# Performance work log

Hardware: AMD Instinct MI355X
Metric: run time of the kernel (lower is better)

## Reference

```python
import jax, jax.numpy as jnp
import numpy as np

N_NODES = 50000
N_EDGES = 1600000
SLOPE = 0.01  # LeakyReLU default negative slope


def _leaky(x):
    return jnp.where(x >= 0, x, SLOPE * x)


def _gcn(x, W, b, row, col, num_nodes):
    """PyG GCNConv: x' = D^{-1/2}(A+I)D^{-1/2} X W + b (self-loops already in row/col)."""
    x = x @ W  # [N, 64]
    deg = jax.ops.segment_sum(jnp.ones_like(row, dtype=x.dtype), col, num_segments=num_nodes)
    dinv = jnp.where(deg > 0, jax.lax.rsqrt(deg), 0.0)
    norm = dinv[row] * dinv[col]  # [E+N]
    msg = x[row] * norm[:, None]  # gather + scale, [E+N, 64]
    out = jax.ops.segment_sum(msg, col, num_segments=num_nodes)
    return out + b


def setup_inputs() -> dict:
    key = jax.random.key(0)
    ks = jax.random.split(key, 24)
    d = {}
    d["screen"] = jax.random.normal(ks[0], (N_NODES, 768), jnp.float32)
    d["des"] = jax.random.normal(ks[1], (N_NODES, 768), jnp.float32)
    d["tweet"] = jax.random.normal(ks[2], (N_NODES, 768), jnp.float32)
    d["profile"] = jax.random.normal(ks[3], (N_NODES, 5), jnp.float32)
    d["personal"] = jax.random.normal(ks[4], (N_NODES, 7), jnp.float32)
    d["edge"] = jax.random.randint(ks[5], (2, N_EDGES), 0, N_NODES, dtype=jnp.int32)

    def lin(k, fan_in, fan_out):
        s = 1.0 / np.sqrt(fan_in)
        k1, k2 = jax.random.split(k)
        W = jax.random.uniform(k1, (fan_in, fan_out), jnp.float32, -s, s)
        b = jax.random.uniform(k2, (fan_out,), jnp.float32, -s, s)
        return W, b

    d["W_screen"], d["b_screen"] = lin(ks[6], 768, 16)
    d["W_des"], d["b_des"] = lin(ks[7], 768, 16)
    d["W_tweet"], d["b_tweet"] = lin(ks[8], 768, 16)
    d["W_pro"], d["b_pro"] = lin(ks[9], 5, 8)
    d["W_per"], d["b_per"] = lin(ks[10], 7, 8)
    d["W_lin"], d["b_lin"] = lin(ks[11], 64, 64)
    d["W_g1"], d["b_g1"] = lin(ks[12], 64, 64)
    d["W_g2"], d["b_g2"] = lin(ks[13], 64, 64)
    d["W_g3"], d["b_g3"] = lin(ks[14], 64, 64)
    d["W_o1"], d["b_o1"] = lin(ks[15], 64, 64)
    d["W_o2"], d["b_o2"] = lin(ks[16], 64, 2)
    return d


def reference(screen, des, tweet, profile, personal, edge,
              W_screen, b_screen, W_des, b_des, W_tweet, b_tweet,
              W_pro, b_pro, W_per, b_per, W_lin, b_lin,
              W_g1, b_g1, W_g2, b_g2, W_g3, b_g3,
              W_o1, b_o1, W_o2, b_o2):
    n = screen.shape[0]
    # dropout layers act as identity in eval mode
    s = _leaky(screen @ W_screen + b_screen)
    de = _leaky(des @ W_des + b_des)
    t = _leaky(tweet @ W_tweet + b_tweet)
    p = _leaky(profile @ W_pro + b_pro)
    pe = _leaky(personal @ W_per + b_per)
    x1 = jnp.concatenate((s, de, t, p, pe), axis=1)  # [N, 64]
    x = _leaky(x1 @ W_lin + b_lin)
    # add self-loops once (shared by all three GCN layers)
    loops = jnp.arange(n, dtype=edge.dtype)
    row = jnp.concatenate([edge[0], loops])
    col = jnp.concatenate([edge[1], loops])
    x = _gcn(x, W_g1, b_g1, row, col, n) + x1
    x = _gcn(x, W_g2, b_g2, row, col, n) + x1
    x = _gcn(x, W_g3, b_g3, row, col, n) + x1
    x = _leaky(x @ W_o1 + b_o1)
    return jax.nn.sigmoid(x @ W_o2 + b_o2)
```

## Files before the change

### kernel.cpp

```cpp
#include <hip/hip_runtime.h>

__device__ __forceinline__ float leaky(float v) { return v >= 0.f ? v : 0.01f * v; }

__device__ __forceinline__ void fma4(float4& a, float s, const float4& w) {
    a.x = fmaf(s, w.x, a.x); a.y = fmaf(s, w.y, a.y);
    a.z = fmaf(s, w.z, a.z); a.w = fmaf(s, w.w, a.w);
}

__device__ __forceinline__ unsigned short f2bf(float x) {
    unsigned b = __float_as_uint(x);
    return (unsigned short)((b + 0x7FFFu + ((b >> 16) & 1u)) >> 16);
}
__device__ __forceinline__ float bf2f(unsigned short u) {
    return __uint_as_float(((unsigned)u) << 16);
}

typedef __attribute__((ext_vector_type(8))) short short8v;
typedef __attribute__((ext_vector_type(4))) float float4v;

__global__ void k_deg(const int* __restrict__ col, int E, int* __restrict__ deg) {
    int e = blockIdx.x * blockDim.x + threadIdx.x;
    if (e < E) atomicAdd(&deg[col[e]], 1);
}

__global__ __launch_bounds__(256) void k_scan_part(const int* __restrict__ deg,
                                                   int* __restrict__ part,
                                                   int* __restrict__ bsum, int N) {
    __shared__ int tmp[256];
    int tid = threadIdx.x;
    int i = blockIdx.x * 256 + tid;
    int v = (i < N) ? deg[i] : 0;
    tmp[tid] = v;
    __syncthreads();
    for (int ofs = 1; ofs < 256; ofs <<= 1) {
        int t = (tid >= ofs) ? tmp[tid - ofs] : 0;
        __syncthreads();
        tmp[tid] += t;
        __syncthreads();
    }
    int incl = tmp[tid];
    if (i < N) part[i] = incl - v;
    if (tid == 255) bsum[blockIdx.x] = incl;
}

__global__ __launch_bounds__(256) void k_scan_sums(const int* __restrict__ bsum,
                                                   int* __restrict__ boff, int NB,
                                                   int* __restrict__ offs_last) {
    __shared__ int tmp[256];
    int tid = threadIdx.x;
    int v = (tid < NB) ? bsum[tid] : 0;
    tmp[tid] = v;
    __syncthreads();
    for (int ofs = 1; ofs < 256; ofs <<= 1) {
        int t = (tid >= ofs) ? tmp[tid - ofs] : 0;
        __syncthreads();
        tmp[tid] += t;
        __syncthreads();
    }
    int incl = tmp[tid];
    if (tid < NB) boff[tid] = incl - v;
    if (tid == 255) offs_last[0] = incl;
}

__global__ __launch_bounds__(256) void k_scan_final(const int* __restrict__ part,
                                                    const int* __restrict__ boff,
                                                    const int* __restrict__ deg,
                                                    int* __restrict__ offs,
                                                    int* __restrict__ pos,
                                                    float* __restrict__ dinv, int N) {
    int i = blockIdx.x * 256 + threadIdx.x;
    if (i < N) {
        int o = part[i] + boff[blockIdx.x];
        offs[i] = o;
        pos[i] = o;
        dinv[i] = rsqrtf((float)(deg[i] + 1));
    }
}

__global__ void k_fill(const int* __restrict__ row, const int* __restrict__ col, int E,
                       int* __restrict__ pos, int* __restrict__ csr) {
    int e = blockIdx.x * blockDim.x + threadIdx.x;
    if (e < E) {
        int p = atomicAdd(&pos[col[e]], 1);
        csr[p] = row[e];
    }
}

__global__ __launch_bounds__(512) void k_featB(
    const float* __restrict__ s, const float* __restrict__ d, const float* __restrict__ t,
    const float* __restrict__ Ws, const float* __restrict__ bs2,
    const float* __restrict__ Wd, const float* __restrict__ bd2,
    const float* __restrict__ Wt, const float* __restrict__ bt2,
    const float* __restrict__ prof, const float* __restrict__ pers,
    const float* __restrict__ Wp, const float* __restrict__ bp,
    const float* __restrict__ Wpe, const float* __restrict__ bpe,
    float* __restrict__ x1g, int N, int NG) {
    __shared__ short8v wfv[3072];

    const int bid = blockIdx.x;
    const int tid = threadIdx.x;

    if (bid >= 3 * NG) {
        int n = (bid - 3 * NG) * 512 + tid;
        if (n >= N) return;
        float pv[5], pe[7];
#pragma unroll
        for (int i = 0; i < 5; ++i) pv[i] = prof[(size_t)n * 5 + i];
#pragma unroll
        for (int i = 0; i < 7; ++i) pe[i] = pers[(size_t)n * 7 + i];
        float o[16];
#pragma unroll
        for (int j = 0; j < 8; ++j) {
            float a = bp[j];
#pragma unroll
            for (int i = 0; i < 5; ++i) a = fmaf(pv[i], Wp[i * 8 + j], a);
            o[j] = leaky(a);
            float a2 = bpe[j];
#pragma unroll
            for (int i = 0; i < 7; ++i) a2 = fmaf(pe[i], Wpe[i * 8 + j], a2);
            o[8 + j] = leaky(a2);
        }
#pragma unroll
        for (int v = 0; v < 4; ++v)
            *reinterpret_cast<float4*>(x1g + (size_t)n * 64 + 48 + v * 4) =
                make_float4(o[v * 4], o[v * 4 + 1], o[v * 4 + 2], o[v * 4 + 3]);
        return;
    }

    const int f = bid / NG;
    const int grp = bid - f * NG;
    const float* __restrict__ X = (f == 0) ? s : ((f == 1) ? d : t);
    const float* __restrict__ W = (f == 0) ? Ws : ((f == 1) ? Wd : Wt);
    const float* __restrict__ B = (f == 0) ? bs2 : ((f == 1) ? bd2 : bt2);
    const int n0 = grp * 128;
    const int lane = tid & 63;
    const int wid = tid >> 6;

    short* wfs = (short*)wfv;
#pragma unroll
    for (int v = 0; v < 6; ++v) {
        int idx4 = tid + v * 512;
        float4 w4 = *reinterpret_cast<const float4*>(W + (size_t)idx4 * 4);
        int k = idx4 >> 2;
        int j0 = (idx4 & 3) * 4;
        int c = k >> 5, g = (k >> 3) & 3, i = k & 7;
        float wq[4] = {w4.x, w4.y, w4.z, w4.w};
#pragma unroll
        for (int q = 0; q < 4; ++q) {
            int sl = (c * 64 + g * 16 + j0 + q) * 8 + i;
            unsigned short h = f2bf(wq[q]);
            wfs[sl] = (short)h;
            wfs[12288 + sl] = (short)f2bf(wq[q] - bf2f(h));
        }
    }
    __syncthreads();

    const int nb = n0 + wid * 16;
    int mrow = nb + (lane & 15); if (mrow >= N) mrow = N - 1;
    const float* base = X + (size_t)mrow * 768 + ((lane >> 4) << 3);

    float4 pa[4], pb[4];
#pragma unroll
    for (int u = 0; u < 4; ++u) {
        pa[u] = *reinterpret_cast<const float4*>(base + u * 32);
        pb[u] = *reinterpret_cast<const float4*>(base + u * 32 + 4);
    }
    float4v acc = {0.f, 0.f, 0.f, 0.f};

#pragma unroll
    for (int c = 0; c < 24; ++c) {
        const int u = c & 3;
        float xs[8] = {pa[u].x, pa[u].y, pa[u].z, pa[u].w,
                       pb[u].x, pb[u].y, pb[u].z, pb[u].w};
        if (c + 4 < 24) {
            pa[u] = *reinterpret_cast<const float4*>(base + (c + 4) * 32);
            pb[u] = *reinterpret_cast<const float4*>(base + (c + 4) * 32 + 4);
        }
        short8v xh, xl;
#pragma unroll
        for (int i = 0; i < 8; ++i) {
            unsigned short h = f2bf(xs[i]);
            xh[i] = (short)h;
            xl[i] = (short)f2bf(xs[i] - bf2f(h));
        }
        short8v wh = wfv[c * 64 + lane];
        short8v wl = wfv[1536 + c * 64 + lane];
        acc = __builtin_amdgcn_mfma_f32_16x16x32_bf16(xh, wh, acc, 0, 0, 0);
        acc = __builtin_amdgcn_mfma_f32_16x16x32_bf16(xl, wh, acc, 0, 0, 0);
        acc = __builtin_amdgcn_mfma_f32_16x16x32_bf16(xh, wl, acc, 0, 0, 0);
    }

    int j = lane & 15;
    float bb = B[j];
#pragma unroll
    for (int r = 0; r < 4; ++r) {
        int n = nb + ((lane >> 4) << 2) + r;
        if (n < N) x1g[(size_t)n * 64 + f * 16 + j] = leaky(acc[r] + bb);
    }
}

__global__ __launch_bounds__(256, 4) void k_mm64(const float* __restrict__ xin,
                                                 const float* __restrict__ W,
                                                 const float* __restrict__ bias,
                                                 const float* __restrict__ dinvv,
                                                 int act, int tobf16,
                                                 void* __restrict__ outp, int N) {
    __shared__ float4 xt4[1024];
    __shared__ float4 wt4[1024];
    const int tid = threadIdx.x;
    const int n0 = blockIdx.x * 64;
#pragma unroll
    for (int v = 0; v < 4; ++v) {
        int L = v * 256 + tid;
        int n = L >> 4, c4 = L & 15;
        int nn = n0 + n; if (nn >= N) nn = N - 1;
        xt4[n * 16 + (c4 ^ (n & 15))] = *reinterpret_cast<const float4*>(xin + (size_t)nn * 64 + c4 * 4);
        wt4[L] = *reinterpret_cast<const float4*>(W + (size_t)L * 4);
    }
    __syncthreads();
    const int nq = tid & 15;
    const int jq = tid >> 4;
    float4 acc[4];
#pragma unroll
    for (int g = 0; g < 4; ++g) acc[g] = make_float4(0.f, 0.f, 0.f, 0.f);
    for (int k = 0; k < 64; k += 4) {
        float4 w0 = wt4[(k + 0) * 16 + jq];
        float4 w1 = wt4[(k + 1) * 16 + jq];
        float4 w2 = wt4[(k + 2) * 16 + jq];
        float4 w3 = wt4[(k + 3) * 16 + jq];
        int k4 = k >> 2;
#pragma unroll
        for (int g = 0; g < 4; ++g) {
            int n = nq + (g << 4);
            float4 xv = xt4[n * 16 + (k4 ^ (n & 15))];
            fma4(acc[g], xv.x, w0);
            fma4(acc[g], xv.y, w1);
            fma4(acc[g], xv.z, w2);
            fma4(acc[g], xv.w, w3);
        }
    }
    float4 bb = make_float4(0.f, 0.f, 0.f, 0.f);
    if (bias) bb = *reinterpret_cast<const float4*>(bias + jq * 4);
#pragma unroll
    for (int g = 0; g < 4; ++g) {
        int n = nq + (g << 4);
        if (n0 + n >= N) continue;
        float4 r = acc[g];
        r.x += bb.x; r.y += bb.y; r.z += bb.z; r.w += bb.w;
        if (act) { r.x = leaky(r.x); r.y = leaky(r.y); r.z = leaky(r.z); r.w = leaky(r.w); }
        if (dinvv) {
            float dv = dinvv[n0 + n];
            r.x *= dv; r.y *= dv; r.z *= dv; r.w *= dv;
        }
        if (tobf16) {
            ushort4 o;
            o.x = f2bf(r.x); o.y = f2bf(r.y); o.z = f2bf(r.z); o.w = f2bf(r.w);
            *reinterpret_cast<ushort4*>((unsigned short*)outp + (size_t)(n0 + n) * 64 + jq * 4) = o;
        } else {
            *reinterpret_cast<float4*>((float*)outp + (size_t)(n0 + n) * 64 + jq * 4) = r;
        }
    }
}

__global__ __launch_bounds__(256) void k_agg(const unsigned short* __restrict__ z,
                                             const int* __restrict__ offs,
                                             const int* __restrict__ csr,
                                             const float* __restrict__ dinv,
                                             const float* __restrict__ bias,
                                             const float* __restrict__ x1,
                                             float* __restrict__ xout, int N) {
    int lane = threadIdx.x & 63;
    int c = blockIdx.x * 4 + (threadIdx.x >> 6);
    if (c >= N) return;
    int s = __builtin_amdgcn_readfirstlane(offs[c]);
    int e = __builtin_amdgcn_readfirstlane(offs[c + 1]);
    const unsigned short* zl = z + lane;
    float acc = bf2f(zl[(size_t)c * 64]);
    float a0 = 0.f, a1 = 0.f, a2 = 0.f, a3 = 0.f;
    float a4 = 0.f, a5 = 0.f, a6 = 0.f, a7 = 0.f;
    int j = s;
    for (; j + 8 <= e; j += 8) {
        int r0 = csr[j + 0], r1 = csr[j + 1], r2 = csr[j + 2], r3 = csr[j + 3];
        int r4 = csr[j + 4], r5 = csr[j + 5], r6 = csr[j + 6], r7 = csr[j + 7];
        a0 += bf2f(zl[(size_t)r0 * 64]);
        a1 += bf2f(zl[(size_t)r1 * 64]);
        a2 += bf2f(zl[(size_t)r2 * 64]);
        a3 += bf2f(zl[(size_t)r3 * 64]);
        a4 += bf2f(zl[(size_t)r4 * 64]);
        a5 += bf2f(zl[(size_t)r5 * 64]);
        a6 += bf2f(zl[(size_t)r6 * 64]);
        a7 += bf2f(zl[(size_t)r7 * 64]);
    }
    for (; j < e; ++j) acc += bf2f(zl[(size_t)csr[j] * 64]);
    acc += ((a0 + a1) + (a2 + a3)) + ((a4 + a5) + (a6 + a7));
    xout[(size_t)c * 64 + lane] = dinv[c] * acc + bias[lane] + x1[(size_t)c * 64 + lane];
}

__global__ __launch_bounds__(256) void k_head(const float* __restrict__ xin,
                                              const float* __restrict__ Wo1,
                                              const float* __restrict__ bo1,
                                              const float* __restrict__ Wo2,
                                              const float* __restrict__ bo2,
                                              float* __restrict__ out, int N) {
    __shared__ float xsg[64][65];
    __shared__ float wg[64][65];
    __shared__ float hs[64][65];
    __shared__ float wo2[128];
    const int tid = threadIdx.x;
    const int n0 = blockIdx.x * 64;
#pragma unroll
    for (int v = 0; v < 4; ++v) {
        int idx = tid + v * 256;
        int n = idx >> 4;
        int jj = (idx & 15) << 2;
        float4 xv = make_float4(0.f, 0.f, 0.f, 0.f);
        if (n0 + n < N) xv = *reinterpret_cast<const float4*>(xin + (size_t)(n0 + n) * 64 + jj);
        xsg[n][jj] = xv.x; xsg[n][jj + 1] = xv.y; xsg[n][jj + 2] = xv.z; xsg[n][jj + 3] = xv.w;
        float4 w = *reinterpret_cast<const float4*>(Wo1 + (size_t)n * 64 + jj);
        wg[n][jj] = w.x; wg[n][jj + 1] = w.y; wg[n][jj + 2] = w.z; wg[n][jj + 3] = w.w;
    }
    if (tid < 128) wo2[tid] = Wo2[tid];
    __syncthreads();
    int j = tid & 63;
    int g = tid >> 6;
    float bj = bo1[j];
    for (int i = 0; i < 16; ++i) {
        int n = g * 16 + i;
        float a = bj;
#pragma unroll
        for (int k = 0; k < 64; ++k) a += xsg[n][k] * wg[k][j];
        hs[n][j] = leaky(a);
    }
    __syncthreads();
    if (tid < 128) {
        int n = tid >> 1;
        int j2 = tid & 1;
        float a = bo2[j2];
#pragma unroll
        for (int k = 0; k < 64; ++k) a += hs[n][k] * wo2[k * 2 + j2];
        if (n0 + n < N) out[(size_t)(n0 + n) * 2 + j2] = 1.f / (1.f + expf(-a));
    }
}

extern "C" void kernel_launch(void* const* d_in, const int* in_sizes, int n_in,
                              void* d_out, int out_size, void* d_ws, size_t ws_size,
                              hipStream_t stream) {
    const float* screen   = (const float*)d_in[0];
    const float* des      = (const float*)d_in[1];
    const float* tweet    = (const float*)d_in[2];
    const float* profile  = (const float*)d_in[3];
    const float* personal = (const float*)d_in[4];
    const int*   edge     = (const int*)d_in[5];
    const float* Ws  = (const float*)d_in[6],  *bs  = (const float*)d_in[7];
    const float* Wd  = (const float*)d_in[8],  *bd  = (const float*)d_in[9];
    const float* Wt  = (const float*)d_in[10], *bt  = (const float*)d_in[11];
    const float* Wp  = (const float*)d_in[12], *bp  = (const float*)d_in[13];
    const float* Wpe = (const float*)d_in[14], *bpe = (const float*)d_in[15];
    const float* Wl  = (const float*)d_in[16], *bl  = (const float*)d_in[17];
    const float* Wg1 = (const float*)d_in[18], *bg1 = (const float*)d_in[19];
    const float* Wg2 = (const float*)d_in[20], *bg2 = (const float*)d_in[21];
    const float* Wg3 = (const float*)d_in[22], *bg3 = (const float*)d_in[23];
    const float* Wo1 = (const float*)d_in[24], *bo1 = (const float*)d_in[25];
    const float* Wo2 = (const float*)d_in[26], *bo2 = (const float*)d_in[27];

    const int N = in_sizes[0] / 768;
    const int E = in_sizes[5] / 2;
    const int* row = edge;
    const int* col = edge + E;

    size_t off = 0;
    auto alloc = [&](size_t bytes) -> void* {
        void* p = (char*)d_ws + off;
        off += (bytes + 255) & ~(size_t)255;
        return p;
    };
    const size_t NF = (size_t)N * 64;
    float* x1   = (float*)alloc(NF * 4);
    float* xa   = (float*)alloc(NF * 4);
    float* xb   = (float*)alloc(NF * 4);
    unsigned short* z = (unsigned short*)alloc(NF * 2);
    float* dinv = (float*)alloc((size_t)N * 4);
    int* deg  = (int*)alloc((size_t)N * 4);
    int* part = (int*)alloc((size_t)N * 4);
    int* offs = (int*)alloc((size_t)(N + 1) * 4);
    int* pos  = (int*)alloc((size_t)N * 4);
    int* csr  = (int*)alloc((size_t)E * 4);
    const int NB = (N + 255) / 256;
    int* bsum = (int*)alloc((size_t)NB * 4);
    int* boff = (int*)alloc((size_t)NB * 4);
    (void)ws_size; (void)n_in; (void)out_size;

    hipMemsetAsync(deg, 0, (size_t)N * 4, stream);
    k_deg<<<(E + 255) / 256, 256, 0, stream>>>(col, E, deg);
    k_scan_part<<<NB, 256, 0, stream>>>(deg, part, bsum, N);
    k_scan_sums<<<1, 256, 0, stream>>>(bsum, boff, NB, offs + N);
    k_scan_final<<<NB, 256, 0, stream>>>(part, boff, deg, offs, pos, dinv, N);
    k_fill<<<(E + 255) / 256, 256, 0, stream>>>(row, col, E, pos, csr);

    const int NG = (N + 127) / 128;
    const int NSM = (N + 511) / 512;
    k_featB<<<NG * 3 + NSM, 512, 0, stream>>>(screen, des, tweet,
                                              Ws, bs, Wd, bd, Wt, bt,
                                              profile, personal, Wp, bp, Wpe, bpe,
                                              x1, N, NG);

    const int NGB = (N + 63) / 64;
    k_mm64<<<NGB, 256, 0, stream>>>(x1, Wl, bl, nullptr, 1, 0, xa, N);

    const int NAB = (N + 3) / 4;
    k_mm64<<<NGB, 256, 0, stream>>>(xa, Wg1, nullptr, dinv, 0, 1, z, N);
    k_agg<<<NAB, 256, 0, stream>>>(z, offs, csr, dinv, bg1, x1, xb, N);
    k_mm64<<<NGB, 256, 0, stream>>>(xb, Wg2, nullptr, dinv, 0, 1, z, N);
    k_agg<<<NAB, 256, 0, stream>>>(z, offs, csr, dinv, bg2, x1, xa, N);
    k_mm64<<<NGB, 256, 0, stream>>>(xa, Wg3, nullptr, dinv, 0, 1, z, N);
    k_agg<<<NAB, 256, 0, stream>>>(z, offs, csr, dinv, bg3, x1, xb, N);

    k_head<<<NGB, 256, 0, stream>>>(xb, Wo1, bo1, Wo2, bo2, (float*)d_out, N);
}
```

Measured before the change: 489.6 us.

## Fuse linear and first GCN matmul; split aggregation across half-waves with packed bf16 loads

The input linear layer (with LeakyReLU) and the first GCN weight matmul now run in one kernel. The intermediate 64-wide activation stays in shared memory instead of going out to global memory and back. The aggregation kernel now has each half-wave process alternate neighbors and read two bf16 values per lane as one 32-bit load, then combines the halves with a lane shuffle. This doubles the neighbor rows in flight per wave, at the cost of divergent tail handling and a cross-lane reduction.

After: 478.9 us. 2.2% less time.

```diff
diff --git a/kernel.cpp b/kernel.cpp
--- a/kernel.cpp
+++ b/kernel.cpp
@@ -199,27 +199,29 @@
     }
 }
 
-__global__ __launch_bounds__(256, 4) void k_mm64(const float* __restrict__ xin,
-                                                 const float* __restrict__ W,
-                                                 const float* __restrict__ bias,
-                                                 const float* __restrict__ dinvv,
-                                                 int act, int tobf16,
-                                                 void* __restrict__ outp, int N) {
+__global__ __launch_bounds__(256) void k_lin1(const float* __restrict__ x1,
+                                              const float* __restrict__ Wl,
+                                              const float* __restrict__ bl,
+                                              const float* __restrict__ Wg1,
+                                              const float* __restrict__ dinvv,
+                                              unsigned short* __restrict__ z, int N) {
     __shared__ float4 xt4[1024];
     __shared__ float4 wt4[1024];
     const int tid = threadIdx.x;
     const int n0 = blockIdx.x * 64;
+    const int nq = tid & 15;
+    const int jq = tid >> 4;
+
 #pragma unroll
     for (int v = 0; v < 4; ++v) {
         int L = v * 256 + tid;
         int n = L >> 4, c4 = L & 15;
         int nn = n0 + n; if (nn >= N) nn = N - 1;
-        xt4[n * 16 + (c4 ^ (n & 15))] = *reinterpret_cast<const float4*>(xin + (size_t)nn * 64 + c4 * 4);
-        wt4[L] = *reinterpret_cast<const float4*>(W + (size_t)L * 4);
-    }
-    __syncthreads();
-    const int nq = tid & 15;
-    const int jq = tid >> 4;
+        xt4[n * 16 + (c4 ^ (n & 15))] = *reinterpret_cast<const float4*>(x1 + (size_t)nn * 64 + c4 * 4);
+        wt4[L] = *reinterpret_cast<const float4*>(Wl + (size_t)L * 4);
+    }
+    __syncthreads();
+
     float4 acc[4];
 #pragma unroll
     for (int g = 0; g < 4; ++g) acc[g] = make_float4(0.f, 0.f, 0.f, 0.f);
@@ -239,26 +241,103 @@
             fma4(acc[g], xv.w, w3);
         }
     }
-    float4 bb = make_float4(0.f, 0.f, 0.f, 0.f);
-    if (bias) bb = *reinterpret_cast<const float4*>(bias + jq * 4);
+    float4 bb = *reinterpret_cast<const float4*>(bl + jq * 4);
+    __syncthreads();
+
+#pragma unroll
+    for (int g = 0; g < 4; ++g) {
+        int n = nq + (g << 4);
+        float4 h;
+        h.x = leaky(acc[g].x + bb.x);
+        h.y = leaky(acc[g].y + bb.y);
+        h.z = leaky(acc[g].z + bb.z);
+        h.w = leaky(acc[g].w + bb.w);
+        xt4[n * 16 + (jq ^ (n & 15))] = h;
+    }
+#pragma unroll
+    for (int v = 0; v < 4; ++v) {
+        int L = v * 256 + tid;
+        wt4[L] = *reinterpret_cast<const float4*>(Wg1 + (size_t)L * 4);
+    }
+    __syncthreads();
+
+#pragma unroll
+    for (int g = 0; g < 4; ++g) acc[g] = make_float4(0.f, 0.f, 0.f, 0.f);
+    for (int k = 0; k < 64; k += 4) {
+        float4 w0 = wt4[(k + 0) * 16 + jq];
+        float4 w1 = wt4[(k + 1) * 16 + jq];
+        float4 w2 = wt4[(k + 2) * 16 + jq];
+        float4 w3 = wt4[(k + 3) * 16 + jq];
+        int k4 = k >> 2;
+#pragma unroll
+        for (int g = 0; g < 4; ++g) {
+            int n = nq + (g << 4);
+            float4 xv = xt4[n * 16 + (k4 ^ (n & 15))];
+            fma4(acc[g], xv.x, w0);
+            fma4(acc[g], xv.y, w1);
+            fma4(acc[g], xv.z, w2);
+            fma4(acc[g], xv.w, w3);
+        }
+    }
 #pragma unroll
     for (int g = 0; g < 4; ++g) {
         int n = nq + (g << 4);
         if (n0 + n >= N) continue;
-        float4 r = acc[g];
-        r.x += bb.x; r.y += bb.y; r.z += bb.z; r.w += bb.w;
-        if (act) { r.x = leaky(r.x); r.y = leaky(r.y); r.z = leaky(r.z); r.w = leaky(r.w); }
-        if (dinvv) {
-            float dv = dinvv[n0 + n];
-            r.x *= dv; r.y *= dv; r.z *= dv; r.w *= dv;
-        }
-        if (tobf16) {
-            ushort4 o;
-            o.x = f2bf(r.x); o.y = f2bf(r.y); o.z = f2bf(r.z); o.w = f2bf(r.w);
-            *reinterpret_cast<ushort4*>((unsigned short*)outp + (size_t)(n0 + n) * 64 + jq * 4) = o;
-        } else {
-            *reinterpret_cast<float4*>((float*)outp + (size_t)(n0 + n) * 64 + jq * 4) = r;
-        }
+        float dv = dinvv[n0 + n];
+        ushort4 o;
+        o.x = f2bf(acc[g].x * dv); o.y = f2bf(acc[g].y * dv);
+        o.z = f2bf(acc[g].z * dv); o.w = f2bf(acc[g].w * dv);
+        *reinterpret_cast<ushort4*>(z + (size_t)(n0 + n) * 64 + jq * 4) = o;
+    }
+}
+
+__global__ __launch_bounds__(256, 4) void k_mm64(const float* __restrict__ xin,
+                                                 const float* __restrict__ W,
+                                                 const float* __restrict__ dinvv,
+                                                 unsigned short* __restrict__ z, int N) {
+    __shared__ float4 xt4[1024];
+    __shared__ float4 wt4[1024];
+    const int tid = threadIdx.x;
+    const int n0 = blockIdx.x * 64;
+#pragma unroll
+    for (int v = 0; v < 4; ++v) {
+        int L = v * 256 + tid;
+        int n = L >> 4, c4 = L & 15;
+        int nn = n0 + n; if (nn >= N) nn = N - 1;
+        xt4[n * 16 + (c4 ^ (n & 15))] = *reinterpret_cast<const float4*>(xin + (size_t)nn * 64 + c4 * 4);
+        wt4[L] = *reinterpret_cast<const float4*>(W + (size_t)L * 4);
+    }
+    __syncthreads();
+    const int nq = tid & 15;
+    const int jq = tid >> 4;
+    float4 acc[4];
+#pragma unroll
+    for (int g = 0; g < 4; ++g) acc[g] = make_float4(0.f, 0.f, 0.f, 0.f);
+    for (int k = 0; k < 64; k += 4) {
+        float4 w0 = wt4[(k + 0) * 16 + jq];
+        float4 w1 = wt4[(k + 1) * 16 + jq];
+        float4 w2 = wt4[(k + 2) * 16 + jq];
+        float4 w3 = wt4[(k + 3) * 16 + jq];
+        int k4 = k >> 2;
+#pragma unroll
+        for (int g = 0; g < 4; ++g) {
+            int n = nq + (g << 4);
+            float4 xv = xt4[n * 16 + (k4 ^ (n & 15))];
+            fma4(acc[g], xv.x, w0);
+            fma4(acc[g], xv.y, w1);
+            fma4(acc[g], xv.z, w2);
+            fma4(acc[g], xv.w, w3);
+        }
+    }
+#pragma unroll
+    for (int g = 0; g < 4; ++g) {
+        int n = nq + (g << 4);
+        if (n0 + n >= N) continue;
+        float dv = dinvv[n0 + n];
+        ushort4 o;
+        o.x = f2bf(acc[g].x * dv); o.y = f2bf(acc[g].y * dv);
+        o.z = f2bf(acc[g].z * dv); o.w = f2bf(acc[g].w * dv);
+        *reinterpret_cast<ushort4*>(z + (size_t)(n0 + n) * 64 + jq * 4) = o;
     }
 }
 
@@ -274,26 +353,57 @@
     if (c >= N) return;
     int s = __builtin_amdgcn_readfirstlane(offs[c]);
     int e = __builtin_amdgcn_readfirstlane(offs[c + 1]);
-    const unsigned short* zl = z + lane;
-    float acc = bf2f(zl[(size_t)c * 64]);
-    float a0 = 0.f, a1 = 0.f, a2 = 0.f, a3 = 0.f;
-    float a4 = 0.f, a5 = 0.f, a6 = 0.f, a7 = 0.f;
+    const int half = lane >> 5;
+    const int d = lane & 31;
+    const unsigned* __restrict__ zr = (const unsigned*)z;
+
+    float ax = 0.f, ay = 0.f;
+    if (half == 0) {
+        unsigned sv = zr[(size_t)c * 32 + d];
+        ax = bf2f((unsigned short)(sv & 0xffffu));
+        ay = bf2f((unsigned short)(sv >> 16));
+    }
+    float ux[8] = {0, 0, 0, 0, 0, 0, 0, 0};
+    float uy[8] = {0, 0, 0, 0, 0, 0, 0, 0};
     int j = s;
-    for (; j + 8 <= e; j += 8) {
-        int r0 = csr[j + 0], r1 = csr[j + 1], r2 = csr[j + 2], r3 = csr[j + 3];
-        int r4 = csr[j + 4], r5 = csr[j + 5], r6 = csr[j + 6], r7 = csr[j + 7];
-        a0 += bf2f(zl[(size_t)r0 * 64]);
-        a1 += bf2f(zl[(size_t)r1 * 64]);
-        a2 += bf2f(zl[(size_t)r2 * 64]);
-        a3 += bf2f(zl[(size_t)r3 * 64]);
-        a4 += bf2f(zl[(size_t)r4 * 64]);
-        a5 += bf2f(zl[(size_t)r5 * 64]);
-        a6 += bf2f(zl[(size_t)r6 * 64]);
-        a7 += bf2f(zl[(size_t)r7 * 64]);
-    }
-    for (; j < e; ++j) acc += bf2f(zl[(size_t)csr[j] * 64]);
-    acc += ((a0 + a1) + (a2 + a3)) + ((a4 + a5) + (a6 + a7));
-    xout[(size_t)c * 64 + lane] = dinv[c] * acc + bias[lane] + x1[(size_t)c * 64 + lane];
+    for (; j + 16 <= e; j += 16) {
+#pragma unroll
+        for (int u = 0; u < 8; ++u) {
+            int r0 = csr[j + 2 * u];
+            int r1 = csr[j + 2 * u + 1];
+            int r = half ? r1 : r0;
+            unsigned v = zr[(size_t)r * 32 + d];
+            ux[u] += bf2f((unsigned short)(v & 0xffffu));
+            uy[u] += bf2f((unsigned short)(v >> 16));
+        }
+    }
+    for (; j + 2 <= e; j += 2) {
+        int r0 = csr[j];
+        int r1 = csr[j + 1];
+        int r = half ? r1 : r0;
+        unsigned v = zr[(size_t)r * 32 + d];
+        ax += bf2f((unsigned short)(v & 0xffffu));
+        ay += bf2f((unsigned short)(v >> 16));
+    }
+    if (j < e && half == 0) {
+        int r = csr[j];
+        unsigned v = zr[(size_t)r * 32 + d];
+        ax += bf2f((unsigned short)(v & 0xffffu));
+        ay += bf2f((unsigned short)(v >> 16));
+    }
+    float tx = ax + ((ux[0] + ux[1]) + (ux[2] + ux[3])) + ((ux[4] + ux[5]) + (ux[6] + ux[7]));
+    float ty = ay + ((uy[0] + uy[1]) + (uy[2] + uy[3])) + ((uy[4] + uy[5]) + (uy[6] + uy[7]));
+    tx += __shfl_xor(tx, 32);
+    ty += __shfl_xor(ty, 32);
+    if (half == 0) {
+        float dv = dinv[c];
+        float2 bb = reinterpret_cast<const float2*>(bias)[d];
+        float2 xx = *reinterpret_cast<const float2*>(x1 + (size_t)c * 64 + 2 * d);
+        float2 o;
+        o.x = dv * tx + bb.x + xx.x;
+        o.y = dv * ty + bb.y + xx.y;
+        *reinterpret_cast<float2*>(xout + (size_t)c * 64 + 2 * d) = o;
+    }
 }
 
 __global__ __launch_bounds__(256) void k_head(const float* __restrict__ xin,
@@ -405,14 +515,12 @@
                                               x1, N, NG);
 
     const int NGB = (N + 63) / 64;
-    k_mm64<<<NGB, 256, 0, stream>>>(x1, Wl, bl, nullptr, 1, 0, xa, N);
-
     const int NAB = (N + 3) / 4;
-    k_mm64<<<NGB, 256, 0, stream>>>(xa, Wg1, nullptr, dinv, 0, 1, z, N);
+    k_lin1<<<NGB, 256, 0, stream>>>(x1, Wl, bl, Wg1, dinv, z, N);
     k_agg<<<NAB, 256, 0, stream>>>(z, offs, csr, dinv, bg1, x1, xb, N);
-    k_mm64<<<NGB, 256, 0, stream>>>(xb, Wg2, nullptr, dinv, 0, 1, z, N);
+    k_mm64<<<NGB, 256, 0, stream>>>(xb, Wg2, dinv, z, N);
     k_agg<<<NAB, 256, 0, stream>>>(z, offs, csr, dinv, bg2, x1, xa, N);
-    k_mm64<<<NGB, 256, 0, stream>>>(xa, Wg3, nullptr, dinv, 0, 1, z, N);
+    k_mm64<<<NGB, 256, 0, stream>>>(xa, Wg3, dinv, z, N);
     k_agg<<<NAB, 256, 0, stream>>>(z, offs, csr, dinv, bg3, x1, xb, N);
 
     k_head<<<NGB, 256, 0, stream>>>(xb, Wo1, bo1, Wo2, bo2, (float*)d_out, N);
```
